# Kernel tuning notes

Measured on AMD Instinct MI355X. Metric: run time of the kernel, lower is better.

## Reference

```python
import jax, jax.numpy as jnp
import numpy as np

EPS = 1e-5
M = 8          # num_modules
NUM_LAYERS = 4


def gumbel_softmax(logits, u, tau):
    g = -jnp.log(-jnp.log(jnp.clip(u, 1e-10, 1.0 - 1e-7)))
    return jax.nn.softmax((logits + g) / tau, axis=-1)


def batchnorm(x, gamma, beta):
    # training-mode BN over batch axis 0; x: [B, ...], gamma/beta broadcast over trailing dims
    mean = jnp.mean(x, axis=0, keepdims=True)
    var = jnp.mean(jnp.square(x - mean), axis=0, keepdims=True)  # biased var, as torch BN
    return (x - mean) * jax.lax.rsqrt(var + EPS) * gamma + beta


def setup_inputs() -> dict:
    key = jax.random.key(0)
    ks = jax.random.split(key, 32)
    B = 16384
    d = {}
    d['x'] = jax.random.normal(ks[0], (B, 128), jnp.float32)
    d['embedding_input'] = jax.random.normal(ks[1], (B, 128), jnp.float32)
    d['u_sel'] = jax.random.uniform(ks[2], (B, NUM_LAYERS - 1, M, M), jnp.float32)
    d['u_final'] = jax.random.uniform(ks[3], (B, M), jnp.float32)
    shapes = [('base_W0', (128, 400)), ('base_b0', (400,)), ('base_W1', (400, 256)), ('base_b1', (256,)),
              ('em_W0', (128, 400)), ('em_b0', (400,)),
              ('gat_W0', (400, 256)), ('gat_b0', (256,)), ('gat_W1', (256, 256)), ('gat_b1', (256,)),
              ('sel_W', (3, 256, 64)), ('sel_b', (3, 64)), ('selF_W', (256, 8)), ('selF_b', (8,)),
              ('cond_W', (3, 64, 256)), ('cond_b', (3, 256)),
              ('mod_W', (8, 256, 256)), ('mod_b', (8, 256)),
              ('last_W', (256, 18)), ('last_b', (18,))]
    for i, (name, sh) in enumerate(shapes):
        fan_in = sh[-2] if len(sh) >= 2 else sh[-1]
        d[name] = jax.random.normal(ks[4 + i], sh, jnp.float32) / np.sqrt(fan_in)
    d['bn1_g'] = jnp.ones((8, 256), jnp.float32)
    d['bn1_b'] = jnp.zeros((8, 256), jnp.float32)
    d['bn2_g'] = jnp.ones((8, 256), jnp.float32)
    d['bn2_b'] = jnp.zeros((8, 256), jnp.float32)
    return d


def forward(x, embedding_input, u_sel, u_final,
            base_W0, base_b0, base_W1, base_b1, em_W0, em_b0,
            gat_W0, gat_b0, gat_W1, gat_b1,
            sel_W, sel_b, selF_W, selF_b, cond_W, cond_b,
            mod_W, mod_b, bn1_g, bn1_b, bn2_g, bn2_b, last_W, last_b):
    relu = jax.nn.relu
    # base MLP (last activation is identity)
    h = relu(x @ base_W0 + base_b0)
    out = h @ base_W1 + base_b1                       # [B, 256]
    # embedding base (single layer, identity last activation)
    emb = embedding_input @ em_W0 + em_b0             # [B, 400]
    # gating fcs: activation THEN fc, per source loop
    emb = relu(emb) @ gat_W0 + gat_b0
    emb = relu(emb) @ gat_W1 + gat_b1                 # [B, 256]

    # routing logits (stochastic branch, tau = select_temp = 1.0)
    select_input = relu(emb)
    gsels = []
    for i in range(NUM_LAYERS - 1):
        logit = jnp.tanh(select_input @ sel_W[i] + sel_b[i])       # [B, 64]
        sraw = logit.reshape(logit.shape[0], M, M)                  # [B, M, M]
        gsels.append(gumbel_softmax(sraw, u_sel[:, i], 1.0))
        select_input = relu((logit @ cond_W[i] + cond_b[i]) * emb)
    final_select = gumbel_softmax(select_input @ selF_W + selF_b, u_final, 1.0)  # [B, M]
    # selects were insert(0, ...)'d in torch -> consumed in reversed order
    selects = gsels[::-1]

    # layer-0 expert modules: BN -> Linear -> BN (only layers[0] is used in forward)
    mean = jnp.mean(out, axis=0, keepdims=True)
    var = jnp.mean(jnp.square(out - mean), axis=0, keepdims=True)
    xhat = (out - mean) * jax.lax.rsqrt(var + EPS)                  # shared normalization
    t = xhat[:, None, :] * bn1_g + bn1_b                            # [B, M, 256] per-module affine
    h = jnp.einsum('bmd,mdh->bmh', t, mod_W) + mod_b                # [B, M, 256]
    prev = batchnorm(h, bn2_g, bn2_b)                               # [B, M, 256]

    # cascade: weighted combination + relu per layer
    for l in range(NUM_LAYERS - 1):
        prev = relu(jnp.einsum('bmk,bkh->bmh', selects[l], prev))
    out = jnp.einsum('bm,bmh->bh', final_select, prev)              # [B, 256]
    return out @ last_W + last_b                                    # [B, 18]


def reference(x, embedding_input, u_sel, u_final,
              base_W0, base_b0, base_W1, base_b1, em_W0, em_b0,
              gat_W0, gat_b0, gat_W1, gat_b1,
              sel_W, sel_b, selF_W, selF_b, cond_W, cond_b,
              mod_W, mod_b, bn1_g, bn1_b, bn2_g, bn2_b, last_W, last_b):
    return forward(x, embedding_input, u_sel, u_final,
                   base_W0, base_b0, base_W1, base_b1, em_W0, em_b0,
                   gat_W0, gat_b0, gat_W1, gat_b1,
                   sel_W, sel_b, selF_W, selF_b, cond_W, cond_b,
                   mod_W, mod_b, bn1_g, bn1_b, bn2_g, bn2_b, last_W, last_b)
```

## Files before the change

kernel.cpp:

```cpp
#include <hip/hip_runtime.h>
#include <math.h>


#define EPI_NONE  0
#define EPI_RELU  1
#define EPI_TANH  2
#define EPI_COND  3
#define EPI_STATS 4

typedef short bf16x8 __attribute__((ext_vector_type(8)));
typedef float f32x4 __attribute__((ext_vector_type(4)));

__device__ __forceinline__ unsigned short f2bf(float f) {
  unsigned u = __float_as_uint(f);
  u += 0x7fffu + ((u >> 16) & 1u);
  return (unsigned short)(u >> 16);
}
__device__ __forceinline__ float bf2f(unsigned short h) {
  return __uint_as_float(((unsigned)h) << 16);
}
__device__ __forceinline__ void gload_lds16(const void* g, void* l) {
  __builtin_amdgcn_global_load_lds(
      (const __attribute__((address_space(1))) unsigned int*)g,
      (__attribute__((address_space(3))) unsigned int*)l, 16, 0, 0);
}
__device__ __forceinline__ bf16x8 relu_bf8(bf16x8 v) {
  bf16x8 r;
  #pragma unroll
  for (int j = 0; j < 8; ++j) r[j] = v[j] > 0 ? v[j] : (short)0;
  return r;
}

__global__ __launch_bounds__(256) void prep_all(
    const float* __restrict__ x, const float* __restrict__ embi,
    const float* __restrict__ base_W0, const float* __restrict__ em_W0,
    const float* __restrict__ base_W1, const float* __restrict__ gat_W0,
    const float* __restrict__ gat_W1, const float* __restrict__ sel_W,
    const float* __restrict__ cond_W, const float* __restrict__ last_W,
    unsigned short* __restrict__ x_bf, unsigned short* __restrict__ e_bf,
    unsigned short* __restrict__ W0t, unsigned short* __restrict__ emW0t,
    unsigned short* __restrict__ W1t, unsigned short* __restrict__ g0t,
    unsigned short* __restrict__ g1t, unsigned short* __restrict__ selWt,
    unsigned short* __restrict__ condWt, float* __restrict__ lastWt,
    float* __restrict__ stats)
{
  __shared__ float t[32][33];
  int bid = blockIdx.x;
  const int tid = threadIdx.x;

  if (bid < 4096) {
    const float* src = bid < 2048 ? x : embi;
    unsigned short* dst = bid < 2048 ? x_bf : e_bf;
    const int i = ((bid & 2047) * 256 + tid) * 4;
    const float4 v = *reinterpret_cast<const float4*>(&src[i]);
    ushort4 o;
    o.x = f2bf(v.x); o.y = f2bf(v.y); o.z = f2bf(v.z); o.w = f2bf(v.w);
    *reinterpret_cast<ushort4*>(&dst[i]) = o;
    return;
  }
  bid -= 4096;

  const int tx = tid & 31, ty = tid >> 5;

  if (bid < 496) {
    const float* src; unsigned short* dst; int K, N, KP, gx, local;
    if (bid < 64)       { src = base_W0; dst = W0t;   K = 128; N = 400; KP = 128; gx = 4;  local = bid; }
    else if (bid < 128) { src = em_W0;   dst = emW0t; K = 128; N = 400; KP = 128; gx = 4;  local = bid - 64; }
    else if (bid < 232) { src = base_W1; dst = W1t;   K = 400; N = 256; KP = 416; gx = 13; local = bid - 128; }
    else if (bid < 336) { src = gat_W0;  dst = g0t;   K = 400; N = 256; KP = 416; gx = 13; local = bid - 232; }
    else if (bid < 400) { src = gat_W1;  dst = g1t;   K = 256; N = 256; KP = 256; gx = 8;  local = bid - 336; }
    else if (bid < 448) {
      const int i = (bid - 400) / 16;
      src = sel_W + i * 16384; dst = selWt + i * 16384;
      K = 256; N = 64; KP = 256; gx = 8; local = (bid - 400) % 16;
    } else {
      const int i = (bid - 448) / 16;
      src = cond_W + i * 16384; dst = condWt + i * 16384;
      K = 64; N = 256; KP = 64; gx = 2; local = (bid - 448) % 16;
    }
    const int k0 = (local % gx) * 32, n0 = (local / gx) * 32;
    #pragma unroll
    for (int p = 0; p < 4; ++p) {
      const int k = k0 + ty + p * 8;
      t[ty + p * 8][tx] = (k < K && n0 + tx < N) ? src[(size_t)k * N + n0 + tx] : 0.f;
    }
    __syncthreads();
    #pragma unroll
    for (int p = 0; p < 4; ++p) {
      const int n = n0 + ty + p * 8;
      dst[(size_t)n * KP + k0 + tx] = f2bf(t[tx][ty + p * 8]);
    }
    return;
  }
  bid -= 496;

  if (bid < 8) {
    const int k0 = bid * 32;
    #pragma unroll
    for (int p = 0; p < 4; ++p)
      t[ty + p * 8][tx] = (tx < 18) ? last_W[(size_t)(k0 + ty + p * 8) * 18 + tx] : 0.f;
    __syncthreads();
    #pragma unroll
    for (int p = 0; p < 4; ++p)
      lastWt[(size_t)(ty + p * 8) * 256 + k0 + tx] = t[tx][ty + p * 8];
    return;
  }

  for (int i = tid; i < 4608; i += 256) stats[i] = 0.f;
}

template<int BN, int WM, int WN, int EPI, bool RELU_A>
__global__ __launch_bounds__(256) void gemm_bf16(
    const unsigned short* __restrict__ A, int AS,
    const unsigned short* __restrict__ Wt, const float* __restrict__ bias,
    unsigned short* __restrict__ C, int CS, int Nreal, int NP, int K,
    const unsigned short* __restrict__ emb,
    float* __restrict__ sum, float* __restrict__ sumsq)
{
  constexpr int FRAG_M = 128 / WM / 16;
  constexpr int FRAG_N = BN / WN / 16;
  __shared__ unsigned short As[128 * 32];
  __shared__ unsigned short Bs[BN * 32];
  const int row0 = blockIdx.y * 128;
  const int n0 = blockIdx.x * BN;
  const int tid = threadIdx.x;
  const int wid = tid >> 6, lane = tid & 63;
  const int wr = wid / WN, wc = wid % WN;
  const int arow = tid >> 2;
  const int kcol = (tid & 3) * 8;
  const int lr = lane & 15, lk = (lane >> 4) * 8;
  const int lrow = (lane >> 4) * 4;

  f32x4 acc[FRAG_M][FRAG_N] = {};
  for (int k0 = 0; k0 < K; k0 += 32) {
    gload_lds16(A + (size_t)(row0 + arow) * AS + k0 + kcol, (char*)As + tid * 16);
    gload_lds16(A + (size_t)(row0 + 64 + arow) * AS + k0 + kcol, (char*)As + 4096 + tid * 16);
    gload_lds16(Wt + (size_t)(n0 + arow) * K + k0 + kcol, (char*)Bs + tid * 16);
    if constexpr (BN == 128)
      gload_lds16(Wt + (size_t)(n0 + 64 + arow) * K + k0 + kcol, (char*)Bs + 4096 + tid * 16);
    __syncthreads();
    bf16x8 a[FRAG_M], b[FRAG_N];
    #pragma unroll
    for (int i = 0; i < FRAG_M; ++i) {
      a[i] = *reinterpret_cast<const bf16x8*>(&As[(wr * (128 / WM) + i * 16 + lr) * 32 + lk]);
      if (RELU_A) a[i] = relu_bf8(a[i]);
    }
    #pragma unroll
    for (int j = 0; j < FRAG_N; ++j)
      b[j] = *reinterpret_cast<const bf16x8*>(&Bs[(wc * (BN / WN) + j * 16 + lr) * 32 + lk]);
    #pragma unroll
    for (int i = 0; i < FRAG_M; ++i)
      #pragma unroll
      for (int j = 0; j < FRAG_N; ++j)
        acc[i][j] = __builtin_amdgcn_mfma_f32_16x16x32_bf16(a[i], b[j], acc[i][j], 0, 0, 0);
    __syncthreads();
  }
  #pragma unroll
  for (int j = 0; j < FRAG_N; ++j) {
    const int col = n0 + wc * (BN / WN) + j * 16 + lr;
    if (col >= NP) continue;
    const bool real = col < Nreal;
    const float bv = real ? bias[col] : 0.f;
    float s = 0.f, q = 0.f;
    #pragma unroll
    for (int i = 0; i < FRAG_M; ++i) {
      #pragma unroll
      for (int r = 0; r < 4; ++r) {
        const int row = row0 + wr * (128 / WM) + i * 16 + lrow + r;
        float v = acc[i][j][r] + bv;
        if (EPI == EPI_RELU) v = fmaxf(v, 0.f);
        if (EPI == EPI_TANH) v = tanhf(v);
        if (EPI == EPI_COND) { v *= bf2f(emb[(size_t)row * 256 + col]); v = fmaxf(v, 0.f); }
        if (!real) v = 0.f;
        const unsigned short hv = f2bf(v);
        C[(size_t)row * CS + col] = hv;
        if (EPI == EPI_STATS) {
          const float vr = bf2f(hv);
          s += vr;
          q = fmaf(vr, vr, q);
        }
      }
    }
    if (EPI == EPI_STATS) {
      s += __shfl_xor(s, 16); s += __shfl_xor(s, 32);
      q += __shfl_xor(q, 16); q += __shfl_xor(q, 32);
      if (lane < 16) {
        atomicAdd(&sum[col], s);
        atomicAdd(&sumsq[col], q);
      }
    }
  }
}

__global__ void gumbel8(const unsigned short* __restrict__ logit, const float* __restrict__ u,
                        float* __restrict__ out, int u_off, int u_stride)
{
  const int idx = blockIdx.x * 256 + threadIdx.x;
  const int b = idx >> 3, m = idx & 7;
  const unsigned short* lp = logit + (size_t)b * 64 + m * 8;
  const float* up = u + (size_t)b * u_stride + u_off + m * 8;
  float v[8];
  #pragma unroll
  for (int j = 0; j < 8; ++j) {
    const float uu = fminf(fmaxf(up[j], 1e-10f), 0.9999999f);
    v[j] = bf2f(lp[j]) - logf(-logf(uu));
  }
  float mx = v[0];
  #pragma unroll
  for (int j = 1; j < 8; ++j) mx = fmaxf(mx, v[j]);
  float s = 0.f;
  #pragma unroll
  for (int j = 0; j < 8; ++j) { v[j] = expf(v[j] - mx); s += v[j]; }
  const float inv = 1.f / s;
  float* op = out + (size_t)b * 64 + m * 8;
  #pragma unroll
  for (int j = 0; j < 8; ++j) op[j] = v[j] * inv;
}

__global__ void final_select_k(const unsigned short* __restrict__ si, const float* __restrict__ Wf,
                               const float* __restrict__ bias, const float* __restrict__ u,
                               float* __restrict__ fs)
{
  const int idx = blockIdx.x * 256 + threadIdx.x;
  const int b = idx >> 3, j = idx & 7;
  const unsigned short* sp = si + (size_t)b * 256;
  float acc = bias[j];
  for (int k = 0; k < 256; ++k) acc = fmaf(bf2f(sp[k]), Wf[k * 8 + j], acc);
  const float uu = fminf(fmaxf(u[(size_t)b * 8 + j], 1e-10f), 0.9999999f);
  float v = acc - logf(-logf(uu));
  float mx = v;
  #pragma unroll
  for (int d = 1; d < 8; d <<= 1) mx = fmaxf(mx, __shfl_xor(mx, d, 8));
  float e = expf(v - mx);
  float s = e;
  #pragma unroll
  for (int d = 1; d < 8; d <<= 1) s += __shfl_xor(s, d, 8);
  fs[(size_t)b * 8 + j] = e / s;
}

__global__ __launch_bounds__(256) void fold_modw_all(
    const float* __restrict__ W, const float* __restrict__ g1,
    const float* __restrict__ b1, const float* __restrict__ modb,
    const float* __restrict__ sum1, const float* __restrict__ sumsq1,
    unsigned short* __restrict__ Wt, float* __restrict__ bias2)
{
  const float invB = 1.f / 16384.f;
  if (blockIdx.z == 8) {
    if (blockIdx.y != 0) return;
    const int m = blockIdx.x, h = threadIdx.x;
    float acc = modb[m * 256 + h];
    for (int d = 0; d < 256; ++d) {
      const float mean = sum1[d] * invB;
      const float var = sumsq1[d] * invB - mean * mean;
      const float r = rsqrtf(var + 1e-5f);
      const float c = b1[m * 256 + d] - mean * r * g1[m * 256 + d];
      acc = fmaf(c, W[((size_t)m * 256 + d) * 256 + h], acc);
    }
    bias2[m * 256 + h] = acc;
    return;
  }
  __shared__ float t[32][33];
  const int m = blockIdx.z, d0 = blockIdx.y * 32, h0 = blockIdx.x * 32;
  const int tx = threadIdx.x & 31, ty = threadIdx.x >> 5;
  #pragma unroll
  for (int p = 0; p < 4; ++p) {
    const int d = d0 + ty + p * 8;
    const float mean = sum1[d] * invB;
    const float var = sumsq1[d] * invB - mean * mean;
    const float r = rsqrtf(var + 1e-5f);
    t[ty + p * 8][tx] = W[((size_t)m * 256 + d) * 256 + h0 + tx] * r * g1[m * 256 + d];
  }
  __syncthreads();
  #pragma unroll
  for (int p = 0; p < 4; ++p) {
    const int h = h0 + ty + p * 8;
    Wt[((size_t)m * 256 + h) * 256 + d0 + tx] = f2bf(t[tx][ty + p * 8]);
  }
}

__global__ __launch_bounds__(256) void final_cascade(
    const unsigned short* __restrict__ H, const float* __restrict__ sum2,
    const float* __restrict__ sumsq2, const float* __restrict__ g2,
    const float* __restrict__ b2, const float* __restrict__ gs0,
    const float* __restrict__ gs1, const float* __restrict__ gs2,
    const float* __restrict__ fs, const float* __restrict__ lastWt,
    const float* __restrict__ lastb, float* __restrict__ out)
{
  const int wave = threadIdx.x >> 6, lane = threadIdx.x & 63;
  const int b = __builtin_amdgcn_readfirstlane(blockIdx.x * 4 + wave);
  const int c0 = lane << 2;
  const float invB = 1.f / 16384.f;

  float prev[8][4];
  #pragma unroll
  for (int m = 0; m < 8; ++m) {
    const int gc = m * 256 + c0;
    const ushort4 h = *reinterpret_cast<const ushort4*>(&H[(size_t)b * 2048 + gc]);
    const float4 s4 = *reinterpret_cast<const float4*>(&sum2[gc]);
    const float4 q4 = *reinterpret_cast<const float4*>(&sumsq2[gc]);
    const float4 gg = *reinterpret_cast<const float4*>(&g2[gc]);
    const float4 bb = *reinterpret_cast<const float4*>(&b2[gc]);
    const float hv[4] = {bf2f(h.x), bf2f(h.y), bf2f(h.z), bf2f(h.w)};
    const float sv[4] = {s4.x, s4.y, s4.z, s4.w};
    const float qv[4] = {q4.x, q4.y, q4.z, q4.w};
    const float gv[4] = {gg.x, gg.y, gg.z, gg.w};
    const float bv[4] = {bb.x, bb.y, bb.z, bb.w};
    #pragma unroll
    for (int c = 0; c < 4; ++c) {
      const float mean = sv[c] * invB;
      const float var = qv[c] * invB - mean * mean;
      const float sc = rsqrtf(var + 1e-5f) * gv[c];
      prev[m][c] = (hv[c] - mean) * sc + bv[c];
    }
  }

  const float* sel0 = gs2 + (size_t)b * 64;
  const float* sel1 = gs1 + (size_t)b * 64;
  const float* sel2 = gs0 + (size_t)b * 64;
  #pragma unroll
  for (int l = 0; l < 3; ++l) {
    const float* sp = (l == 0) ? sel0 : (l == 1) ? sel1 : sel2;
    float nw[8][4];
    #pragma unroll
    for (int m = 0; m < 8; ++m) {
      float a0 = 0.f, a1 = 0.f, a2 = 0.f, a3 = 0.f;
      #pragma unroll
      for (int k = 0; k < 8; ++k) {
        const float s = sp[m * 8 + k];
        a0 = fmaf(s, prev[k][0], a0);
        a1 = fmaf(s, prev[k][1], a1);
        a2 = fmaf(s, prev[k][2], a2);
        a3 = fmaf(s, prev[k][3], a3);
      }
      nw[m][0] = fmaxf(a0, 0.f); nw[m][1] = fmaxf(a1, 0.f);
      nw[m][2] = fmaxf(a2, 0.f); nw[m][3] = fmaxf(a3, 0.f);
    }
    #pragma unroll
    for (int m = 0; m < 8; ++m)
      #pragma unroll
      for (int c = 0; c < 4; ++c)
        prev[m][c] = nw[m][c];
  }

  const float* fp = fs + (size_t)b * 8;
  float ov[4] = {0.f, 0.f, 0.f, 0.f};
  #pragma unroll
  for (int m = 0; m < 8; ++m) {
    const float s = fp[m];
    ov[0] = fmaf(s, prev[m][0], ov[0]);
    ov[1] = fmaf(s, prev[m][1], ov[1]);
    ov[2] = fmaf(s, prev[m][2], ov[2]);
    ov[3] = fmaf(s, prev[m][3], ov[3]);
  }

  #pragma unroll
  for (int t = 0; t < 18; ++t) {
    const float4 w = *reinterpret_cast<const float4*>(&lastWt[t * 256 + c0]);
    float p = fmaf(ov[0], w.x, fmaf(ov[1], w.y, fmaf(ov[2], w.z, ov[3] * w.w)));
    #pragma unroll
    for (int d = 1; d < 64; d <<= 1) p += __shfl_xor(p, d);
    if (lane == 0) out[(size_t)b * 18 + t] = p + lastb[t];
  }
}

extern "C" void kernel_launch(void* const* d_in, const int* in_sizes, int n_in,
                              void* d_out, int out_size, void* d_ws, size_t ws_size,
                              hipStream_t stream)
{
  (void)in_sizes; (void)n_in; (void)out_size; (void)ws_size;
  const float* x       = (const float*)d_in[0];
  const float* embi    = (const float*)d_in[1];
  const float* u_sel   = (const float*)d_in[2];
  const float* u_fin   = (const float*)d_in[3];
  const float* base_W0 = (const float*)d_in[4];
  const float* base_b0 = (const float*)d_in[5];
  const float* base_W1 = (const float*)d_in[6];
  const float* base_b1 = (const float*)d_in[7];
  const float* em_W0   = (const float*)d_in[8];
  const float* em_b0   = (const float*)d_in[9];
  const float* gat_W0  = (const float*)d_in[10];
  const float* gat_b0  = (const float*)d_in[11];
  const float* gat_W1  = (const float*)d_in[12];
  const float* gat_b1  = (const float*)d_in[13];
  const float* sel_W   = (const float*)d_in[14];
  const float* sel_b   = (const float*)d_in[15];
  const float* selF_W  = (const float*)d_in[16];
  const float* selF_b  = (const float*)d_in[17];
  const float* cond_W  = (const float*)d_in[18];
  const float* cond_b  = (const float*)d_in[19];
  const float* mod_W   = (const float*)d_in[20];
  const float* mod_b   = (const float*)d_in[21];
  const float* last_W  = (const float*)d_in[22];
  const float* last_b  = (const float*)d_in[23];
  const float* bn1_g   = (const float*)d_in[24];
  const float* bn1_b   = (const float*)d_in[25];
  const float* bn2_g   = (const float*)d_in[26];
  const float* bn2_b   = (const float*)d_in[27];

  char* WSB = (char*)d_ws;
  unsigned short* h_big    = (unsigned short*)(WSB + 0);
  unsigned short* h1       = (unsigned short*)(WSB + 67108864);
  unsigned short* x_bf     = (unsigned short*)(WSB + 80740352);
  unsigned short* e_bf     = (unsigned short*)(WSB + 84934656);
  unsigned short* emb_bf   = (unsigned short*)(WSB + 89128960);
  unsigned short* si_bf    = (unsigned short*)(WSB + 97517568);
  unsigned short* out_bf   = (unsigned short*)(WSB + 105906176);
  unsigned short* logit_bf = (unsigned short*)(WSB + 114294784);
  float* gs0   = (float*)(WSB + 116391936);
  float* gs1   = (float*)(WSB + 120586240);
  float* gs2   = (float*)(WSB + 124780544);
  float* bufFs = (float*)(WSB + 128974848);
  unsigned short* W0t   = (unsigned short*)(WSB + 129499136);
  unsigned short* emW0t = (unsigned short*)(WSB + 129630208);
  unsigned short* W1t   = (unsigned short*)(WSB + 129761280);
  unsigned short* g0t   = (unsigned short*)(WSB + 129974272);
  unsigned short* g1t   = (unsigned short*)(WSB + 130187264);
  unsigned short* selWt = (unsigned short*)(WSB + 130318336);
  unsigned short* condWt= (unsigned short*)(WSB + 130416640);
  unsigned short* modWt = (unsigned short*)(WSB + 130514944);
  float* bias2  = (float*)(WSB + 131563520);
  float* stats  = (float*)(WSB + 131571712);
  float* lastWt = (float*)(WSB + 131590144);
  float* sum1   = stats;        float* sumsq1 = stats + 256;
  float* sum2   = stats + 512;  float* sumsq2 = stats + 2560;

  const dim3 blk(256);
  prep_all<<<dim3(4601), blk, 0, stream>>>(
      x, embi, base_W0, em_W0, base_W1, gat_W0, gat_W1, sel_W, cond_W, last_W,
      x_bf, e_bf, W0t, emW0t, W1t, g0t, g1t, selWt, condWt, lastWt, stats);

  gemm_bf16<128, 2, 2, EPI_RELU, false><<<dim3(4, 128), blk, 0, stream>>>(
      x_bf, 128, W0t, base_b0, h1, 416, 400, 416, 128, nullptr, nullptr, nullptr);
  gemm_bf16<128, 2, 2, EPI_STATS, false><<<dim3(2, 128), blk, 0, stream>>>(
      h1, 416, W1t, base_b1, out_bf, 256, 256, 256, 416, nullptr, sum1, sumsq1);
  gemm_bf16<128, 2, 2, EPI_RELU, false><<<dim3(4, 128), blk, 0, stream>>>(
      e_bf, 128, emW0t, em_b0, h1, 416, 400, 416, 128, nullptr, nullptr, nullptr);
  gemm_bf16<128, 2, 2, EPI_RELU, false><<<dim3(2, 128), blk, 0, stream>>>(
      h1, 416, g0t, gat_b0, si_bf, 256, 256, 256, 416, nullptr, nullptr, nullptr);
  gemm_bf16<128, 2, 2, EPI_NONE, false><<<dim3(2, 128), blk, 0, stream>>>(
      si_bf, 256, g1t, gat_b1, emb_bf, 256, 256, 256, 256, nullptr, nullptr, nullptr);
  float* gs[3] = {gs0, gs1, gs2};
  for (int i = 0; i < 3; ++i) {
    if (i == 0)
      gemm_bf16<64, 4, 1, EPI_TANH, true><<<dim3(1, 128), blk, 0, stream>>>(
          emb_bf, 256, selWt, sel_b, logit_bf, 64, 64, 64, 256, nullptr, nullptr, nullptr);
    else
      gemm_bf16<64, 4, 1, EPI_TANH, false><<<dim3(1, 128), blk, 0, stream>>>(
          si_bf, 256, selWt + i * 16384, sel_b + i * 64, logit_bf, 64, 64, 64, 256, nullptr, nullptr, nullptr);
    gumbel8<<<dim3(512), blk, 0, stream>>>(logit_bf, u_sel, gs[i], i * 64, 192);
    gemm_bf16<128, 2, 2, EPI_COND, false><<<dim3(2, 128), blk, 0, stream>>>(
        logit_bf, 64, condWt + i * 16384, cond_b + i * 256, si_bf, 256, 256, 256, 64, emb_bf, nullptr, nullptr);
  }
  final_select_k<<<dim3(512), blk, 0, stream>>>(si_bf, selF_W, selF_b, u_fin, bufFs);
  fold_modw_all<<<dim3(8, 8, 9), blk, 0, stream>>>(
      mod_W, bn1_g, bn1_b, mod_b, sum1, sumsq1, modWt, bias2);
  gemm_bf16<128, 2, 2, EPI_STATS, false><<<dim3(16, 128), blk, 0, stream>>>(
      out_bf, 256, modWt, bias2, h_big, 2048, 2048, 2048, 256, nullptr, sum2, sumsq2);
  final_cascade<<<dim3(4096), blk, 0, stream>>>(
      h_big, sum2, sumsq2, bn2_g, bn2_b, gs0, gs1, gs2, bufFs, lastWt, last_b, (float*)d_out);
}
```

Measured before the change: 289.9 us.

## Move final linear layer to MFMA GEMM and precompute BN2 scale/shift

The per-row 18-output projection in final_cascade used wave-wide shuffle reductions, 18 per row. That work moves to a separate bf16 MFMA GEMM kernel, and final_cascade now writes a bf16 intermediate vector instead. A small kernel also precomputes the BN2 scale and shift, so final_cascade no longer recomputes rsqrt and mean per element. The cost is two extra launches, an extra intermediate round trip through memory, and bf16 rounding of the final-layer inputs and weights.

```diff
diff --git a/kernel.cpp b/kernel.cpp
--- a/kernel.cpp
+++ b/kernel.cpp
@@ -41,7 +41,7 @@
     unsigned short* __restrict__ W0t, unsigned short* __restrict__ emW0t,
     unsigned short* __restrict__ W1t, unsigned short* __restrict__ g0t,
     unsigned short* __restrict__ g1t, unsigned short* __restrict__ selWt,
-    unsigned short* __restrict__ condWt, float* __restrict__ lastWt,
+    unsigned short* __restrict__ condWt, unsigned short* __restrict__ lastWt,
     float* __restrict__ stats)
 {
   __shared__ float t[32][33];
@@ -101,8 +101,11 @@
       t[ty + p * 8][tx] = (tx < 18) ? last_W[(size_t)(k0 + ty + p * 8) * 18 + tx] : 0.f;
     __syncthreads();
     #pragma unroll
-    for (int p = 0; p < 4; ++p)
-      lastWt[(size_t)(ty + p * 8) * 256 + k0 + tx] = t[tx][ty + p * 8];
+    for (int p = 0; p < 4; ++p) {
+      const int n = ty + p * 8;
+      lastWt[(size_t)n * 256 + k0 + tx] = f2bf(t[tx][n]);
+      lastWt[(size_t)(n + 32) * 256 + k0 + tx] = 0;
+    }
     return;
   }
 
@@ -192,6 +195,56 @@
   }
 }
 
+__global__ __launch_bounds__(256) void gemm_last(
+    const unsigned short* __restrict__ A, const unsigned short* __restrict__ Wt,
+    const float* __restrict__ bias, float* __restrict__ out)
+{
+  __shared__ unsigned short As[128 * 32];
+  __shared__ unsigned short Bs[64 * 32];
+  const int row0 = blockIdx.y * 128;
+  const int tid = threadIdx.x;
+  const int wid = tid >> 6, lane = tid & 63;
+  const int arow = tid >> 2;
+  const int kcol = (tid & 3) * 8;
+  const int lr = lane & 15, lk = (lane >> 4) * 8;
+  const int lrow = (lane >> 4) * 4;
+
+  f32x4 acc[2][4] = {};
+  for (int k0 = 0; k0 < 256; k0 += 32) {
+    gload_lds16(A + (size_t)(row0 + arow) * 256 + k0 + kcol, (char*)As + tid * 16);
+    gload_lds16(A + (size_t)(row0 + 64 + arow) * 256 + k0 + kcol, (char*)As + 4096 + tid * 16);
+    gload_lds16(Wt + (size_t)arow * 256 + k0 + kcol, (char*)Bs + tid * 16);
+    __syncthreads();
+    bf16x8 a[2], b[4];
+    #pragma unroll
+    for (int i = 0; i < 2; ++i)
+      a[i] = *reinterpret_cast<const bf16x8*>(&As[(wid * 32 + i * 16 + lr) * 32 + lk]);
+    #pragma unroll
+    for (int j = 0; j < 4; ++j)
+      b[j] = *reinterpret_cast<const bf16x8*>(&Bs[(j * 16 + lr) * 32 + lk]);
+    #pragma unroll
+    for (int i = 0; i < 2; ++i)
+      #pragma unroll
+      for (int j = 0; j < 4; ++j)
+        acc[i][j] = __builtin_amdgcn_mfma_f32_16x16x32_bf16(a[i], b[j], acc[i][j], 0, 0, 0);
+    __syncthreads();
+  }
+  #pragma unroll
+  for (int j = 0; j < 2; ++j) {
+    const int col = j * 16 + lr;
+    if (col >= 18) continue;
+    const float bv = bias[col];
+    #pragma unroll
+    for (int i = 0; i < 2; ++i) {
+      #pragma unroll
+      for (int r = 0; r < 4; ++r) {
+        const int row = row0 + wid * 32 + i * 16 + lrow + r;
+        out[(size_t)row * 18 + col] = acc[i][j][r] + bv;
+      }
+    }
+  }
+}
+
 __global__ void gumbel8(const unsigned short* __restrict__ logit, const float* __restrict__ u,
                         float* __restrict__ out, int u_off, int u_stride)
 {
@@ -278,40 +331,41 @@
   }
 }
 
+__global__ void finalize_bn2(const float* __restrict__ sum, const float* __restrict__ sumsq,
+                             const float* __restrict__ g, const float* __restrict__ b,
+                             float* __restrict__ scale, float* __restrict__ shift)
+{
+  const int i = blockIdx.x * 256 + threadIdx.x;
+  const float invB = 1.f / 16384.f;
+  const float m = sum[i] * invB;
+  const float v = sumsq[i] * invB - m * m;
+  const float r = rsqrtf(v + 1e-5f);
+  const float sc = r * g[i];
+  scale[i] = sc;
+  shift[i] = b[i] - m * sc;
+}
+
 __global__ __launch_bounds__(256) void final_cascade(
-    const unsigned short* __restrict__ H, const float* __restrict__ sum2,
-    const float* __restrict__ sumsq2, const float* __restrict__ g2,
-    const float* __restrict__ b2, const float* __restrict__ gs0,
+    const unsigned short* __restrict__ H, const float* __restrict__ scale2,
+    const float* __restrict__ shift2, const float* __restrict__ gs0,
     const float* __restrict__ gs1, const float* __restrict__ gs2,
-    const float* __restrict__ fs, const float* __restrict__ lastWt,
-    const float* __restrict__ lastb, float* __restrict__ out)
+    const float* __restrict__ fs, unsigned short* __restrict__ ovec)
 {
   const int wave = threadIdx.x >> 6, lane = threadIdx.x & 63;
   const int b = __builtin_amdgcn_readfirstlane(blockIdx.x * 4 + wave);
   const int c0 = lane << 2;
-  const float invB = 1.f / 16384.f;
 
   float prev[8][4];
   #pragma unroll
   for (int m = 0; m < 8; ++m) {
     const int gc = m * 256 + c0;
     const ushort4 h = *reinterpret_cast<const ushort4*>(&H[(size_t)b * 2048 + gc]);
-    const float4 s4 = *reinterpret_cast<const float4*>(&sum2[gc]);
-    const float4 q4 = *reinterpret_cast<const float4*>(&sumsq2[gc]);
-    const float4 gg = *reinterpret_cast<const float4*>(&g2[gc]);
-    const float4 bb = *reinterpret_cast<const float4*>(&b2[gc]);
-    const float hv[4] = {bf2f(h.x), bf2f(h.y), bf2f(h.z), bf2f(h.w)};
-    const float sv[4] = {s4.x, s4.y, s4.z, s4.w};
-    const float qv[4] = {q4.x, q4.y, q4.z, q4.w};
-    const float gv[4] = {gg.x, gg.y, gg.z, gg.w};
-    const float bv[4] = {bb.x, bb.y, bb.z, bb.w};
-    #pragma unroll
-    for (int c = 0; c < 4; ++c) {
-      const float mean = sv[c] * invB;
-      const float var = qv[c] * invB - mean * mean;
-      const float sc = rsqrtf(var + 1e-5f) * gv[c];
-      prev[m][c] = (hv[c] - mean) * sc + bv[c];
-    }
+    const float4 sc = *reinterpret_cast<const float4*>(&scale2[gc]);
+    const float4 sh = *reinterpret_cast<const float4*>(&shift2[gc]);
+    prev[m][0] = bf2f(h.x) * sc.x + sh.x;
+    prev[m][1] = bf2f(h.y) * sc.y + sh.y;
+    prev[m][2] = bf2f(h.z) * sc.z + sh.z;
+    prev[m][3] = bf2f(h.w) * sc.w + sh.w;
   }
 
   const float* sel0 = gs2 + (size_t)b * 64;
@@ -352,15 +406,9 @@
     ov[2] = fmaf(s, prev[m][2], ov[2]);
     ov[3] = fmaf(s, prev[m][3], ov[3]);
   }
-
-  #pragma unroll
-  for (int t = 0; t < 18; ++t) {
-    const float4 w = *reinterpret_cast<const float4*>(&lastWt[t * 256 + c0]);
-    float p = fmaf(ov[0], w.x, fmaf(ov[1], w.y, fmaf(ov[2], w.z, ov[3] * w.w)));
-    #pragma unroll
-    for (int d = 1; d < 64; d <<= 1) p += __shfl_xor(p, d);
-    if (lane == 0) out[(size_t)b * 18 + t] = p + lastb[t];
-  }
+  ushort4 o;
+  o.x = f2bf(ov[0]); o.y = f2bf(ov[1]); o.z = f2bf(ov[2]); o.w = f2bf(ov[3]);
+  *reinterpret_cast<ushort4*>(&ovec[(size_t)b * 256 + c0]) = o;
 }
 
 extern "C" void kernel_launch(void* const* d_in, const int* in_sizes, int n_in,
@@ -400,6 +448,7 @@
   char* WSB = (char*)d_ws;
   unsigned short* h_big    = (unsigned short*)(WSB + 0);
   unsigned short* h1       = (unsigned short*)(WSB + 67108864);
+  unsigned short* ovec_bf  = (unsigned short*)(WSB + 67108864);
   unsigned short* x_bf     = (unsigned short*)(WSB + 80740352);
   unsigned short* e_bf     = (unsigned short*)(WSB + 84934656);
   unsigned short* emb_bf   = (unsigned short*)(WSB + 89128960);
@@ -420,7 +469,9 @@
   unsigned short* modWt = (unsigned short*)(WSB + 130514944);
   float* bias2  = (float*)(WSB + 131563520);
   float* stats  = (float*)(WSB + 131571712);
-  float* lastWt = (float*)(WSB + 131590144);
+  unsigned short* lastWt = (unsigned short*)(WSB + 131590144);
+  float* scale2 = (float*)(WSB + 131622912);
+  float* shift2 = (float*)(WSB + 131631104);
   float* sum1   = stats;        float* sumsq1 = stats + 256;
   float* sum2   = stats + 512;  float* sumsq2 = stats + 2560;
 
@@ -456,6 +507,8 @@
       mod_W, bn1_g, bn1_b, mod_b, sum1, sumsq1, modWt, bias2);
   gemm_bf16<128, 2, 2, EPI_STATS, false><<<dim3(16, 128), blk, 0, stream>>>(
       out_bf, 256, modWt, bias2, h_big, 2048, 2048, 2048, 256, nullptr, sum2, sumsq2);
+  finalize_bn2<<<dim3(8), blk, 0, stream>>>(sum2, sumsq2, bn2_g, bn2_b, scale2, shift2);
   final_cascade<<<dim3(4096), blk, 0, stream>>>(
-      h_big, sum2, sumsq2, bn2_g, bn2_b, gs0, gs1, gs2, bufFs, lastWt, last_b, (float*)d_out);
-}
+      h_big, scale2, shift2, gs0, gs1, gs2, bufFs, ovec_bf);
+  gemm_last<<<dim3(1, 128), blk, 0, stream>>>(ovec_bf, lastWt, last_b, (float*)d_out);
+}
```

After: 268.0 us. 1.08x faster.
